# Performance work log

Measured on AMD Instinct MI355X. Metric: run time of the kernel, lower is better.

Reference implementation:

```python
import jax, jax.numpy as jnp
import numpy as np
import math

D_MODEL = 256
N_HEADS = 8
HEAD_DIM = D_MODEL // N_HEADS  # 32
N_LEVELS = 4
N_POINTS = 4
SHAPES = [(112, 112), (56, 56), (28, 28), (14, 14)]
LEN_IN = sum(h * w for h, w in SHAPES)  # 16660
BATCH = 1
LEN_Q = LEN_IN


def _grid_init_bias():
    # Faithful to MSDeformAttn._reset_parameters: directional grid init for sampling_offsets bias.
    thetas = np.arange(N_HEADS, dtype=np.float32) * (2.0 * math.pi / N_HEADS)
    grid = np.stack([np.cos(thetas), np.sin(thetas)], -1)
    grid = grid / np.abs(grid).max(-1, keepdims=True)
    grid = np.tile(grid[:, None, None, :], (1, N_LEVELS, N_POINTS, 1)).copy()
    for i in range(N_POINTS):
        grid[:, :, i, :] *= i + 1
    return jnp.asarray(grid.reshape(-1), dtype=jnp.float32)


def setup_inputs() -> dict:
    key = jax.random.key(0)
    ks = jax.random.split(key, 10)
    s = 1.0 / math.sqrt(D_MODEL)
    return {
        "query": jax.random.normal(ks[0], (BATCH, LEN_Q, D_MODEL), jnp.float32),
        "reference_points": jax.random.uniform(ks[1], (BATCH, LEN_Q, N_LEVELS, 2), jnp.float32),
        "input_flatten": jax.random.normal(ks[2], (BATCH, LEN_IN, D_MODEL), jnp.float32),
        "spatial_shapes": jnp.asarray(SHAPES, dtype=jnp.int32),
        "level_start_index": jnp.asarray(np.cumsum([0] + [h * w for h, w in SHAPES])[:-1], dtype=jnp.int32),
        "W_q": jax.random.normal(ks[3], (D_MODEL, D_MODEL), jnp.float32) * s,
        "b_q": jnp.zeros((D_MODEL,), jnp.float32),
        "W_k": jax.random.normal(ks[4], (D_MODEL, D_MODEL), jnp.float32) * s,
        "b_k": jnp.zeros((D_MODEL,), jnp.float32),
        "W_v": jax.random.normal(ks[5], (D_MODEL, D_MODEL), jnp.float32) * s,
        "b_v": jnp.zeros((D_MODEL,), jnp.float32),
        "W_o": jax.random.normal(ks[6], (D_MODEL, D_MODEL), jnp.float32) * s,
        "b_o": jnp.zeros((D_MODEL,), jnp.float32),
        "W_off": jax.random.normal(ks[7], (D_MODEL, N_HEADS * N_LEVELS * N_POINTS * 2), jnp.float32) * 0.01,
        "b_off": _grid_init_bias(),
    }


def _bilinear_sample(img, grid, H, W):
    # img: (B, H*W, D) flattened feature map; grid: (B, Q, P, 2) in [-1, 1] (x, y order).
    # Matches F.grid_sample(mode='bilinear', padding_mode='zeros', align_corners=False).
    B, Q, P, _ = grid.shape
    x = ((grid[..., 0] + 1.0) * W - 1.0) * 0.5
    y = ((grid[..., 1] + 1.0) * H - 1.0) * 0.5
    x0 = jnp.floor(x)
    y0 = jnp.floor(y)
    lx = x - x0
    ly = y - y0
    x0i = x0.astype(jnp.int32)
    y0i = y0.astype(jnp.int32)

    def gather(yi, xi, w):
        valid = (xi >= 0) & (xi < W) & (yi >= 0) & (yi < H)
        idx = jnp.clip(yi, 0, H - 1) * W + jnp.clip(xi, 0, W - 1)
        v = jnp.take_along_axis(img, idx.reshape(B, Q * P, 1), axis=1)
        return v.reshape(B, Q, P, -1) * (w * valid)[..., None]

    return (gather(y0i, x0i, (1.0 - ly) * (1.0 - lx))
            + gather(y0i, x0i + 1, (1.0 - ly) * lx)
            + gather(y0i + 1, x0i, ly * (1.0 - lx))
            + gather(y0i + 1, x0i + 1, ly * lx))


def reference(query, reference_points, input_flatten, spatial_shapes, level_start_index,
              W_q, b_q, W_k, b_k, W_v, b_v, W_o, b_o, W_off, b_off):
    N, Lq, C = query.shape
    M, D, L, P = N_HEADS, HEAD_DIM, N_LEVELS, N_POINTS

    q = query @ W_q + b_q                                   # (N, Lq, C)
    value = (input_flatten @ W_v + b_v).reshape(N, -1, M, D)
    key_h = (input_flatten @ W_k + b_k).reshape(N, -1, M, D)

    offsets = (q @ W_off + b_off).reshape(N, Lq, M, L, P, 2)
    # offset_normalizer = (W_l, H_l) per level
    norm = jnp.stack([spatial_shapes[:, 1], spatial_shapes[:, 0]], -1).astype(q.dtype)
    loc = reference_points[:, :, None, :, None, :] + offsets / norm[None, None, None, :, None, :]
    grids = 2.0 * loc - 1.0                                  # (N, Lq, M, L, P, 2)

    samp_v, samp_k = [], []
    start = 0
    for lid, (H, W) in enumerate(SHAPES):
        end = start + H * W
        v_l = value[:, start:end].transpose(0, 2, 1, 3).reshape(N * M, H * W, D)
        k_l = key_h[:, start:end].transpose(0, 2, 1, 3).reshape(N * M, H * W, D)
        g_l = grids[:, :, :, lid].transpose(0, 2, 1, 3, 4).reshape(N * M, Lq, P, 2)
        samp_v.append(_bilinear_sample(v_l, g_l, H, W))      # (N*M, Lq, P, D)
        samp_k.append(_bilinear_sample(k_l, g_l, H, W))
        start = end

    v_s = jnp.stack(samp_v, axis=2).reshape(N, M, Lq, L, P, D)
    k_s = jnp.stack(samp_k, axis=2).reshape(N, M, Lq, L, P, D)

    qh = q.reshape(N, Lq, M, D)
    logits = jnp.einsum('nqmd,nmqlpd->nmqlp', qh, k_s) / math.sqrt(D)
    attn = jax.nn.softmax(logits.reshape(N, M, Lq, L * P), axis=-1).reshape(N, M, Lq, L, P)

    out = jnp.einsum('nmqlp,nmqlpd->nqmd', attn, v_s).reshape(N, Lq, C)
    return out @ W_o + b_o
```

## Files before the change

kernel.cpp:

```cpp
#include <hip/hip_runtime.h>
#include <hip/hip_bf16.h>
#include <math.h>

#define LEN_IN   16660
#define D_MODEL  256
#define N_HEADS  8

typedef __attribute__((ext_vector_type(8))) short short8v;
typedef __attribute__((ext_vector_type(4))) float f32x4;
typedef _Float16 f16x2 __attribute__((ext_vector_type(2)));
typedef _Float16 f16x8 __attribute__((ext_vector_type(8)));

__device__ __forceinline__ unsigned short f2h(float f) {
  union { unsigned short u; _Float16 h; } c;
  c.h = (_Float16)f;
  return c.u;
}
__device__ __forceinline__ float h2f(unsigned short u) {
  union { unsigned short u; _Float16 h; } c;
  c.u = u;
  return (float)c.h;
}
__device__ __forceinline__ f16x2 u2h(unsigned u) {
  union { unsigned u; f16x2 h; } c;
  c.u = u;
  return c.h;
}

__global__ __launch_bounds__(256) void mega_prep(
    const float* __restrict__ query, const float* __restrict__ inp,
    const float* __restrict__ Wq, const float* __restrict__ Wk,
    const float* __restrict__ Wv, const float* __restrict__ Woff,
    const float* __restrict__ Wo,
    const float* __restrict__ bq, const float* __restrict__ boff,
    unsigned short* __restrict__ q16, unsigned short* __restrict__ in16,
    unsigned short* __restrict__ Btq, unsigned short* __restrict__ Btk,
    unsigned short* __restrict__ Btv, unsigned short* __restrict__ Bto,
    unsigned short* __restrict__ Btqo, float* __restrict__ bqo) {
  int b = blockIdx.x;
  int tid = threadIdx.x;

  if (b < 2048) {
    const int nq = (LEN_IN * D_MODEL) / 4;
    int i = b * 256 + tid;
    const int stride = 2048 * 256;
    for (int qd = i; qd < nq; qd += stride) {
      float4 va = ((const float4*)query)[qd];
      ushort4 ha = {f2h(va.x), f2h(va.y), f2h(va.z), f2h(va.w)};
      ((ushort4*)q16)[qd] = ha;
      float4 vb = ((const float4*)inp)[qd];
      ushort4 hb = {f2h(vb.x), f2h(vb.y), f2h(vb.z), f2h(vb.w)};
      ((ushort4*)in16)[qd] = hb;
    }
    return;
  }

  if (b < 2128) {
    __shared__ float tile[64][65];
    int bb = b - 2048;
    int mat = bb >> 4, t = bb & 15;
    int ti = t >> 2, tj = t & 3;
    const float* W = (mat == 0) ? Wq : (mat == 1) ? Wk : (mat == 2) ? Wv
                   : (mat == 3) ? Woff : Wo;
    unsigned short* Bt = (mat == 0) ? Btq : (mat == 1) ? Btk : (mat == 2) ? Btv
                       : (mat == 3) ? nullptr : Bto;
    if (mat == 3) return;
    #pragma unroll
    for (int i = 0; i < 16; i++) {
      int idx = tid + i * 256;
      int kr = idx >> 6, nc = idx & 63;
      tile[kr][nc] = W[(size_t)(ti * 64 + kr) * 256 + tj * 64 + nc];
    }
    __syncthreads();
    #pragma unroll
    for (int i = 0; i < 16; i++) {
      int idx = tid + i * 256;
      int nr = idx >> 6, kc = idx & 63;
      Bt[(size_t)(tj * 64 + nr) * 256 + ti * 64 + kc] = f2h(tile[kc][nr]);
    }
    return;
  }

  if (b == 2128) {
    float s = boff[tid];
    for (int i = 0; i < 256; i++) s += bq[i] * Woff[(size_t)i * 256 + tid];
    bqo[tid] = s;
    return;
  }

  {
    const int P = 40;
    __shared__ short As[64 * P], Bs[64 * P];
    int t = b - 2129;
    int m0 = (t >> 2) * 64, n0 = (t & 3) * 64;
    int w = tid >> 6, l = tid & 63;
    int r = l & 15, g = l >> 4;
    int mi = (w >> 1) * 32, ni = (w & 1) * 32;
    int sm = tid >> 2, sp = tid & 3;
    int kr = tid >> 3, nc = (tid & 7) * 8;

    f32x4 acc[2][2];
    #pragma unroll
    for (int a = 0; a < 2; a++)
      #pragma unroll
      for (int c = 0; c < 2; c++) acc[a][c] = (f32x4){0.f, 0.f, 0.f, 0.f};

    for (int k0 = 0; k0 < 256; k0 += 32) {
      const float* src = Wq + (size_t)(m0 + sm) * 256 + k0 + sp * 8;
      float4 u0 = *(const float4*)src;
      float4 u1 = *(const float4*)(src + 4);
      f16x8 hv = {(_Float16)u0.x, (_Float16)u0.y, (_Float16)u0.z, (_Float16)u0.w,
                  (_Float16)u1.x, (_Float16)u1.y, (_Float16)u1.z, (_Float16)u1.w};
      *(f16x8*)&As[sm * P + sp * 8] = hv;
      const float* wsrc = Woff + (size_t)(k0 + kr) * 256 + n0 + nc;
      float4 w0 = *(const float4*)wsrc;
      float4 w1 = *(const float4*)(wsrc + 4);
      Bs[(nc + 0) * P + kr] = (short)f2h(w0.x);
      Bs[(nc + 1) * P + kr] = (short)f2h(w0.y);
      Bs[(nc + 2) * P + kr] = (short)f2h(w0.z);
      Bs[(nc + 3) * P + kr] = (short)f2h(w0.w);
      Bs[(nc + 4) * P + kr] = (short)f2h(w1.x);
      Bs[(nc + 5) * P + kr] = (short)f2h(w1.y);
      Bs[(nc + 6) * P + kr] = (short)f2h(w1.z);
      Bs[(nc + 7) * P + kr] = (short)f2h(w1.w);
      __syncthreads();
      f16x8 af[2], bf[2];
      #pragma unroll
      for (int a = 0; a < 2; a++)
        af[a] = *(f16x8*)&As[(mi + a * 16 + r) * P + g * 8];
      #pragma unroll
      for (int c = 0; c < 2; c++)
        bf[c] = *(f16x8*)&Bs[(ni + c * 16 + r) * P + g * 8];
      #pragma unroll
      for (int a = 0; a < 2; a++)
        #pragma unroll
        for (int c = 0; c < 2; c++)
          acc[a][c] = __builtin_amdgcn_mfma_f32_16x16x32_f16(af[a], bf[c], acc[a][c], 0, 0, 0);
      __syncthreads();
    }
    #pragma unroll
    for (int a = 0; a < 2; a++)
      #pragma unroll
      for (int c = 0; c < 2; c++) {
        int col = n0 + ni + c * 16 + r;
        #pragma unroll
        for (int i = 0; i < 4; i++) {
          int row = m0 + mi + a * 16 + g * 4 + i;
          Btqo[(size_t)col * 256 + row] = f2h(acc[a][c][i]);
        }
      }
  }
}

__global__ __launch_bounds__(256) void gemm_qkv(
    const unsigned short* __restrict__ q16, const unsigned short* __restrict__ in16,
    const unsigned short* __restrict__ Btq,
    const unsigned short* __restrict__ Btk,
    const unsigned short* __restrict__ Btv,
    const unsigned short* __restrict__ Btqo,
    const float* __restrict__ bq, const float* __restrict__ bk,
    const float* __restrict__ bv, const float* __restrict__ bqo,
    unsigned short* __restrict__ qp_out, unsigned* __restrict__ kv_out,
    unsigned short* __restrict__ offs_out, int M) {
  const int P = 72;
  __shared__ short As[128 * P], B1[64 * P], B2[64 * P];
  int z = blockIdx.z;
  const unsigned short* A = (z == 1) ? in16 : q16;
  const unsigned short* Bt1 = (z == 0) ? Btq : (z == 1) ? Btk : Btqo;
  int tid = threadIdx.x;
  int m0 = blockIdx.x * 128, n0 = blockIdx.y * 64;
  int w = tid >> 6, l = tid & 63;
  int r = l & 15, g = l >> 4;
  int mi = (w >> 1) * 64, ni = (w & 1) * 32;
  int arow = tid >> 1, ach = (tid & 1) * 32;
  int brow = tid >> 2, bch = (tid & 3) * 16;

  f32x4 acc1[4][2], acc2[4][2];
  #pragma unroll
  for (int a = 0; a < 4; a++)
    #pragma unroll
    for (int b = 0; b < 2; b++) {
      acc1[a][b] = (f32x4){0.f, 0.f, 0.f, 0.f};
      acc2[a][b] = (f32x4){0.f, 0.f, 0.f, 0.f};
    }

  for (int k0 = 0; k0 < 256; k0 += 64) {
    int gm = m0 + arow;
    short8v a0 = {0,0,0,0,0,0,0,0}, a1 = a0, a2 = a0, a3 = a0;
    if (gm < M) {
      const unsigned short* src = A + (size_t)gm * 256 + k0 + ach;
      a0 = *(const short8v*)src;
      a1 = *(const short8v*)(src + 8);
      a2 = *(const short8v*)(src + 16);
      a3 = *(const short8v*)(src + 24);
    }
    *(short8v*)&As[arow * P + ach] = a0;
    *(short8v*)&As[arow * P + ach + 8] = a1;
    *(short8v*)&As[arow * P + ach + 16] = a2;
    *(short8v*)&As[arow * P + ach + 24] = a3;
    {
      const unsigned short* bsrc = Bt1 + (size_t)(n0 + brow) * 256 + k0 + bch;
      *(short8v*)&B1[brow * P + bch] = *(const short8v*)bsrc;
      *(short8v*)&B1[brow * P + bch + 8] = *(const short8v*)(bsrc + 8);
    }
    if (z == 1) {
      const unsigned short* bsrc = Btv + (size_t)(n0 + brow) * 256 + k0 + bch;
      *(short8v*)&B2[brow * P + bch] = *(const short8v*)bsrc;
      *(short8v*)&B2[brow * P + bch + 8] = *(const short8v*)(bsrc + 8);
    }
    __syncthreads();

    f16x8 af[4][2], b1f[2][2], b2f[2][2];
    #pragma unroll
    for (int a = 0; a < 4; a++)
      #pragma unroll
      for (int ks = 0; ks < 2; ks++)
        af[a][ks] = *(f16x8*)&As[(mi + a * 16 + r) * P + ks * 32 + g * 8];
    #pragma unroll
    for (int b = 0; b < 2; b++)
      #pragma unroll
      for (int ks = 0; ks < 2; ks++)
        b1f[b][ks] = *(f16x8*)&B1[(ni + b * 16 + r) * P + ks * 32 + g * 8];
    if (z == 1) {
      #pragma unroll
      for (int b = 0; b < 2; b++)
        #pragma unroll
        for (int ks = 0; ks < 2; ks++)
          b2f[b][ks] = *(f16x8*)&B2[(ni + b * 16 + r) * P + ks * 32 + g * 8];
    }
    #pragma unroll
    for (int a = 0; a < 4; a++)
      #pragma unroll
      for (int b = 0; b < 2; b++)
        #pragma unroll
        for (int ks = 0; ks < 2; ks++) {
          acc1[a][b] = __builtin_amdgcn_mfma_f32_16x16x32_f16(af[a][ks], b1f[b][ks], acc1[a][b], 0, 0, 0);
          if (z == 1)
            acc2[a][b] = __builtin_amdgcn_mfma_f32_16x16x32_f16(af[a][ks], b2f[b][ks], acc2[a][b], 0, 0, 0);
        }
    __syncthreads();
  }

  #pragma unroll
  for (int a = 0; a < 4; a++)
    #pragma unroll
    for (int b = 0; b < 2; b++) {
      int col = n0 + ni + b * 16 + r;
      if (z == 0) {
        float bc = bq[col];
        #pragma unroll
        for (int i = 0; i < 4; i++) {
          int row = m0 + mi + a * 16 + g * 4 + i;
          if (row < M) qp_out[(size_t)row * 256 + col] = f2h(acc1[a][b][i] + bc);
        }
      } else if (z == 1) {
        float bkc = bk[col], bvc = bv[col];
        int hh = col >> 5, cc = col & 31;
        #pragma unroll
        for (int i = 0; i < 4; i++) {
          int row = m0 + mi + a * 16 + g * 4 + i;
          if (row < M) {
            unsigned kh = f2h(acc1[a][b][i] + bkc);
            unsigned vh = f2h(acc2[a][b][i] + bvc);
            kv_out[((size_t)hh * LEN_IN + row) * 32 + cc] = kh | (vh << 16);
          }
        }
      } else {
        float bc = bqo[col];
        #pragma unroll
        for (int i = 0; i < 4; i++) {
          int row = m0 + mi + a * 16 + g * 4 + i;
          if (row < M) offs_out[(size_t)row * 256 + col] = f2h(acc1[a][b][i] + bc);
        }
      }
    }
}

__global__ __launch_bounds__(256) void gemm_out(
    const unsigned short* __restrict__ A,
    const unsigned short* __restrict__ Bt,
    const float* __restrict__ bias, float* __restrict__ C, int M) {
  const int P = 72;
  __shared__ short As[128 * P], Bs[64 * P];
  int tid = threadIdx.x;
  int m0 = blockIdx.x * 128, n0 = blockIdx.y * 64;
  int w = tid >> 6, l = tid & 63;
  int r = l & 15, g = l >> 4;
  int mi = (w >> 1) * 64, ni = (w & 1) * 32;
  int arow = tid >> 1, ach = (tid & 1) * 32;
  int brow = tid >> 2, bch = (tid & 3) * 16;

  f32x4 acc[4][2];
  #pragma unroll
  for (int a = 0; a < 4; a++)
    #pragma unroll
    for (int b = 0; b < 2; b++) acc[a][b] = (f32x4){0.f, 0.f, 0.f, 0.f};

  for (int k0 = 0; k0 < 256; k0 += 64) {
    int gm = m0 + arow;
    short8v a0 = {0,0,0,0,0,0,0,0}, a1 = a0, a2 = a0, a3 = a0;
    if (gm < M) {
      const unsigned short* src = A + (size_t)gm * 256 + k0 + ach;
      a0 = *(const short8v*)src;
      a1 = *(const short8v*)(src + 8);
      a2 = *(const short8v*)(src + 16);
      a3 = *(const short8v*)(src + 24);
    }
    *(short8v*)&As[arow * P + ach] = a0;
    *(short8v*)&As[arow * P + ach + 8] = a1;
    *(short8v*)&As[arow * P + ach + 16] = a2;
    *(short8v*)&As[arow * P + ach + 24] = a3;
    const unsigned short* bsrc = Bt + (size_t)(n0 + brow) * 256 + k0 + bch;
    *(short8v*)&Bs[brow * P + bch] = *(const short8v*)bsrc;
    *(short8v*)&Bs[brow * P + bch + 8] = *(const short8v*)(bsrc + 8);
    __syncthreads();

    f16x8 af[4][2], bf[2][2];
    #pragma unroll
    for (int a = 0; a < 4; a++)
      #pragma unroll
      for (int ks = 0; ks < 2; ks++)
        af[a][ks] = *(f16x8*)&As[(mi + a * 16 + r) * P + ks * 32 + g * 8];
    #pragma unroll
    for (int b = 0; b < 2; b++)
      #pragma unroll
      for (int ks = 0; ks < 2; ks++)
        bf[b][ks] = *(f16x8*)&Bs[(ni + b * 16 + r) * P + ks * 32 + g * 8];
    #pragma unroll
    for (int a = 0; a < 4; a++)
      #pragma unroll
      for (int b = 0; b < 2; b++)
        #pragma unroll
        for (int ks = 0; ks < 2; ks++)
          acc[a][b] = __builtin_amdgcn_mfma_f32_16x16x32_f16(af[a][ks], bf[b][ks], acc[a][b], 0, 0, 0);
    __syncthreads();
  }
  #pragma unroll
  for (int a = 0; a < 4; a++)
    #pragma unroll
    for (int b = 0; b < 2; b++) {
      int col = n0 + ni + b * 16 + r;
      float bc = bias[col];
      #pragma unroll
      for (int i = 0; i < 4; i++) {
        int row = m0 + mi + a * 16 + g * 4 + i;
        if (row < M) C[(size_t)row * 256 + col] = acc[a][b][i] + bc;
      }
    }
}

__global__ __launch_bounds__(256) void sample_attn(
    const unsigned short* __restrict__ qp,
    const unsigned short* __restrict__ offs,
    const float* __restrict__ rp,
    const unsigned* __restrict__ kv,
    unsigned short* __restrict__ attn_out) {
  __shared__ float vbuf[4][16][36];

  int tid = threadIdx.x;
  int wslot = tid >> 6;
  int lane = tid & 63;
  int wid = blockIdx.x * 4 + wslot;
  int q = wid >> 3;
  int h = wid & 7;

  int pt = lane >> 2;
  int c8 = (lane & 3) * 8;
  int l5 = lane & 31;

  float offv = h2f(offs[(size_t)q * 256 + h * 32 + l5]);
  float rpv = (l5 < 8) ? rp[(size_t)q * 8 + l5] : 0.f;

  int l = pt >> 2, pp = pt & 3;
  int W = 112 >> l;
  int start = (int)((50176u - (50176u >> (2 * l))) / 3u);

  float off_x = __shfl(offv, l * 8 + pp * 2 + 0, 32);
  float off_y = __shfl(offv, l * 8 + pp * 2 + 1, 32);
  float rp_x = __shfl(rpv, l * 2 + 0, 32);
  float rp_y = __shfl(rpv, l * 2 + 1, 32);

  float x = rp_x * (float)W + off_x - 0.5f;
  float y = rp_y * (float)W + off_y - 0.5f;
  float x0f = floorf(x), y0f = floorf(y);
  float lx = x - x0f, ly = y - y0f;
  int x0 = (int)x0f, y0 = (int)y0f;
  float wx0 = 1.f - lx, wy0 = 1.f - ly;
  float tw[4] = {wy0 * wx0, wy0 * lx, ly * wx0, ly * lx};

  const unsigned* kvh = kv + (size_t)h * LEN_IN * 32 + c8;

  f16x2 acc[8];
  #pragma unroll
  for (int j = 0; j < 8; j++) acc[j] = (f16x2){(_Float16)0.f, (_Float16)0.f};

  #pragma unroll
  for (int tap = 0; tap < 4; tap++) {
    int yy = y0 + (tap >> 1), xx = x0 + (tap & 1);
    bool valid = ((unsigned)xx < (unsigned)W) & ((unsigned)yy < (unsigned)W);
    float wgt = valid ? tw[tap] : 0.f;
    int pix = valid ? (start + yy * W + xx) : start;
    const unsigned* p = kvh + (size_t)pix * 32;
    uint4 u0 = *(const uint4*)p;
    uint4 u1 = *(const uint4*)(p + 4);
    _Float16 wh = (_Float16)wgt;
    f16x2 w2 = {wh, wh};
    acc[0] += w2 * u2h(u0.x);
    acc[1] += w2 * u2h(u0.y);
    acc[2] += w2 * u2h(u0.z);
    acc[3] += w2 * u2h(u0.w);
    acc[4] += w2 * u2h(u1.x);
    acc[5] += w2 * u2h(u1.y);
    acc[6] += w2 * u2h(u1.z);
    acc[7] += w2 * u2h(u1.w);
  }

  uint4 qa = *(const uint4*)(qp + (size_t)q * 256 + h * 32 + c8);
  float dot = 0.f;
  f16x2 kp;
  kp[0] = acc[0][0]; kp[1] = acc[1][0];
  dot = __builtin_amdgcn_fdot2(u2h(qa.x), kp, dot, false);
  kp[0] = acc[2][0]; kp[1] = acc[3][0];
  dot = __builtin_amdgcn_fdot2(u2h(qa.y), kp, dot, false);
  kp[0] = acc[4][0]; kp[1] = acc[5][0];
  dot = __builtin_amdgcn_fdot2(u2h(qa.z), kp, dot, false);
  kp[0] = acc[6][0]; kp[1] = acc[7][0];
  dot = __builtin_amdgcn_fdot2(u2h(qa.w), kp, dot, false);
  dot += __shfl_xor(dot, 1, 64);
  dot += __shfl_xor(dot, 2, 64);

  float e = __expf(dot * 0.17677669529663687f);
  float s = e;
  s += __shfl_xor(s, 4, 64);
  s += __shfl_xor(s, 8, 64);
  s += __shfl_xor(s, 16, 64);
  s += __shfl_xor(s, 32, 64);
  float wsc = e / s;

  float4 v0 = {wsc * (float)acc[0][1], wsc * (float)acc[1][1],
               wsc * (float)acc[2][1], wsc * (float)acc[3][1]};
  float4 v1 = {wsc * (float)acc[4][1], wsc * (float)acc[5][1],
               wsc * (float)acc[6][1], wsc * (float)acc[7][1]};
  *(float4*)&vbuf[wslot][pt][c8] = v0;
  *(float4*)&vbuf[wslot][pt][c8 + 4] = v1;
  __syncthreads();

  if (lane < 32) {
    float o = 0.f;
    #pragma unroll
    for (int p = 0; p < 16; p++) o += vbuf[wslot][p][lane];
    attn_out[(size_t)q * 256 + h * 32 + lane] = f2h(o);
  }
}

extern "C" void kernel_launch(void* const* d_in, const int* in_sizes, int n_in,
                              void* d_out, int out_size, void* d_ws, size_t ws_size,
                              hipStream_t stream) {
  const float* query = (const float*)d_in[0];
  const float* rp    = (const float*)d_in[1];
  const float* inp   = (const float*)d_in[2];
  const float* W_q   = (const float*)d_in[5];
  const float* b_q   = (const float*)d_in[6];
  const float* W_k   = (const float*)d_in[7];
  const float* b_k   = (const float*)d_in[8];
  const float* W_v   = (const float*)d_in[9];
  const float* b_v   = (const float*)d_in[10];
  const float* W_o   = (const float*)d_in[11];
  const float* b_o   = (const float*)d_in[12];
  const float* W_off = (const float*)d_in[13];
  const float* b_off = (const float*)d_in[14];
  float* out = (float*)d_out;

  const size_t nelem = (size_t)LEN_IN * D_MODEL;
  unsigned short* q16   = (unsigned short*)d_ws;
  unsigned short* in16  = q16 + nelem;
  unsigned short* qp    = in16 + nelem;
  unsigned short* offsb = qp + nelem;
  unsigned short* attn  = offsb + nelem;
  unsigned* kvp = (unsigned*)(attn + nelem);
  unsigned short* Btq   = (unsigned short*)(kvp + nelem);
  unsigned short* Btk   = Btq + 256 * 256;
  unsigned short* Btv   = Btk + 256 * 256;
  unsigned short* Bto   = Btv + 256 * 256;
  unsigned short* Btqo  = Bto + 256 * 256;
  float* bqo = (float*)(Btqo + 256 * 256);

  dim3 blk(256);
  dim3 ggrid((LEN_IN + 127) / 128, D_MODEL / 64);
  dim3 ggrid3((LEN_IN + 127) / 128, D_MODEL / 64, 3);

  mega_prep<<<2145, blk, 0, stream>>>(query, inp, W_q, W_k, W_v, W_off, W_o,
                                      b_q, b_off, q16, in16,
                                      Btq, Btk, Btv, Bto, Btqo, bqo);

  gemm_qkv<<<ggrid3, blk, 0, stream>>>(q16, in16, Btq, Btk, Btv, Btqo,
                                       b_q, b_k, b_v, bqo,
                                       qp, kvp, offsb, LEN_IN);

  int n_blocks = LEN_IN * N_HEADS / 4;
  sample_attn<<<n_blocks, blk, 0, stream>>>(qp, offsb, rp, kvp, attn);

  gemm_out<<<ggrid, blk, 0, stream>>>(attn, Bto, b_o, out, LEN_IN);
}
```

Measured before the change: 119.7 us.

## Fuse query fp16 conversion into GEMM and merge Q/offset projections

Drops the separate query fp32-to-fp16 conversion pass. The query tile is now loaded as fp32 and converted while it is staged into shared memory inside the GEMM. The Q and fused offset projections now share one A tile per block (z=0 computes both), so the grid shrinks from three z-slices to two and redundant A loads are removed. The sampling kernel also remaps block indices across queries and spreads the final 16-point reduction over all 64 lanes with a shuffle. In exchange, the z=0 blocks read twice as many bytes of A from global memory.

```diff
diff --git a/kernel.cpp b/kernel.cpp
--- a/kernel.cpp
+++ b/kernel.cpp
@@ -28,12 +28,12 @@
 }
 
 __global__ __launch_bounds__(256) void mega_prep(
-    const float* __restrict__ query, const float* __restrict__ inp,
+    const float* __restrict__ inp,
     const float* __restrict__ Wq, const float* __restrict__ Wk,
     const float* __restrict__ Wv, const float* __restrict__ Woff,
     const float* __restrict__ Wo,
     const float* __restrict__ bq, const float* __restrict__ boff,
-    unsigned short* __restrict__ q16, unsigned short* __restrict__ in16,
+    unsigned short* __restrict__ in16,
     unsigned short* __restrict__ Btq, unsigned short* __restrict__ Btk,
     unsigned short* __restrict__ Btv, unsigned short* __restrict__ Bto,
     unsigned short* __restrict__ Btqo, float* __restrict__ bqo) {
@@ -45,9 +45,6 @@
     int i = b * 256 + tid;
     const int stride = 2048 * 256;
     for (int qd = i; qd < nq; qd += stride) {
-      float4 va = ((const float4*)query)[qd];
-      ushort4 ha = {f2h(va.x), f2h(va.y), f2h(va.z), f2h(va.w)};
-      ((ushort4*)q16)[qd] = ha;
       float4 vb = ((const float4*)inp)[qd];
       ushort4 hb = {f2h(vb.x), f2h(vb.y), f2h(vb.z), f2h(vb.w)};
       ((ushort4*)in16)[qd] = hb;
@@ -60,11 +57,9 @@
     int bb = b - 2048;
     int mat = bb >> 4, t = bb & 15;
     int ti = t >> 2, tj = t & 3;
-    const float* W = (mat == 0) ? Wq : (mat == 1) ? Wk : (mat == 2) ? Wv
-                   : (mat == 3) ? Woff : Wo;
-    unsigned short* Bt = (mat == 0) ? Btq : (mat == 1) ? Btk : (mat == 2) ? Btv
-                       : (mat == 3) ? nullptr : Bto;
     if (mat == 3) return;
+    const float* W = (mat == 0) ? Wq : (mat == 1) ? Wk : (mat == 2) ? Wv : Wo;
+    unsigned short* Bt = (mat == 0) ? Btq : (mat == 1) ? Btk : (mat == 2) ? Btv : Bto;
     #pragma unroll
     for (int i = 0; i < 16; i++) {
       int idx = tid + i * 256;
@@ -153,7 +148,7 @@
 }
 
 __global__ __launch_bounds__(256) void gemm_qkv(
-    const unsigned short* __restrict__ q16, const unsigned short* __restrict__ in16,
+    const float* __restrict__ queryF, const unsigned short* __restrict__ in16,
     const unsigned short* __restrict__ Btq,
     const unsigned short* __restrict__ Btk,
     const unsigned short* __restrict__ Btv,
@@ -165,8 +160,8 @@
   const int P = 72;
   __shared__ short As[128 * P], B1[64 * P], B2[64 * P];
   int z = blockIdx.z;
-  const unsigned short* A = (z == 1) ? in16 : q16;
-  const unsigned short* Bt1 = (z == 0) ? Btq : (z == 1) ? Btk : Btqo;
+  const unsigned short* Bt1 = (z == 0) ? Btq : Btk;
+  const unsigned short* Bt2 = (z == 0) ? Btqo : Btv;
   int tid = threadIdx.x;
   int m0 = blockIdx.x * 128, n0 = blockIdx.y * 64;
   int w = tid >> 6, l = tid & 63;
@@ -186,27 +181,40 @@
 
   for (int k0 = 0; k0 < 256; k0 += 64) {
     int gm = m0 + arow;
-    short8v a0 = {0,0,0,0,0,0,0,0}, a1 = a0, a2 = a0, a3 = a0;
-    if (gm < M) {
-      const unsigned short* src = A + (size_t)gm * 256 + k0 + ach;
-      a0 = *(const short8v*)src;
-      a1 = *(const short8v*)(src + 8);
-      a2 = *(const short8v*)(src + 16);
-      a3 = *(const short8v*)(src + 24);
-    }
-    *(short8v*)&As[arow * P + ach] = a0;
-    *(short8v*)&As[arow * P + ach + 8] = a1;
-    *(short8v*)&As[arow * P + ach + 16] = a2;
-    *(short8v*)&As[arow * P + ach + 24] = a3;
+    if (z == 0) {
+      #pragma unroll
+      for (int t = 0; t < 4; t++) {
+        f16x8 hv = {0, 0, 0, 0, 0, 0, 0, 0};
+        if (gm < M) {
+          const float* src = queryF + (size_t)gm * 256 + k0 + ach + t * 8;
+          float4 u0 = *(const float4*)src;
+          float4 u1 = *(const float4*)(src + 4);
+          hv = (f16x8){(_Float16)u0.x, (_Float16)u0.y, (_Float16)u0.z, (_Float16)u0.w,
+                       (_Float16)u1.x, (_Float16)u1.y, (_Float16)u1.z, (_Float16)u1.w};
+        }
+        *(f16x8*)&As[arow * P + ach + t * 8] = hv;
+      }
+    } else {
+      short8v a0 = {0,0,0,0,0,0,0,0}, a1 = a0, a2 = a0, a3 = a0;
+      if (gm < M) {
+        const unsigned short* src = in16 + (size_t)gm * 256 + k0 + ach;
+        a0 = *(const short8v*)src;
+        a1 = *(const short8v*)(src + 8);
+        a2 = *(const short8v*)(src + 16);
+        a3 = *(const short8v*)(src + 24);
+      }
+      *(short8v*)&As[arow * P + ach] = a0;
+      *(short8v*)&As[arow * P + ach + 8] = a1;
+      *(short8v*)&As[arow * P + ach + 16] = a2;
+      *(short8v*)&As[arow * P + ach + 24] = a3;
+    }
     {
       const unsigned short* bsrc = Bt1 + (size_t)(n0 + brow) * 256 + k0 + bch;
       *(short8v*)&B1[brow * P + bch] = *(const short8v*)bsrc;
       *(short8v*)&B1[brow * P + bch + 8] = *(const short8v*)(bsrc + 8);
-    }
-    if (z == 1) {
-      const unsigned short* bsrc = Btv + (size_t)(n0 + brow) * 256 + k0 + bch;
-      *(short8v*)&B2[brow * P + bch] = *(const short8v*)bsrc;
-      *(short8v*)&B2[brow * P + bch + 8] = *(const short8v*)(bsrc + 8);
+      const unsigned short* bsrc2 = Bt2 + (size_t)(n0 + brow) * 256 + k0 + bch;
+      *(short8v*)&B2[brow * P + bch] = *(const short8v*)bsrc2;
+      *(short8v*)&B2[brow * P + bch + 8] = *(const short8v*)(bsrc2 + 8);
     }
     __syncthreads();
 
@@ -219,15 +227,10 @@
     #pragma unroll
     for (int b = 0; b < 2; b++)
       #pragma unroll
-      for (int ks = 0; ks < 2; ks++)
+      for (int ks = 0; ks < 2; ks++) {
         b1f[b][ks] = *(f16x8*)&B1[(ni + b * 16 + r) * P + ks * 32 + g * 8];
-    if (z == 1) {
-      #pragma unroll
-      for (int b = 0; b < 2; b++)
-        #pragma unroll
-        for (int ks = 0; ks < 2; ks++)
-          b2f[b][ks] = *(f16x8*)&B2[(ni + b * 16 + r) * P + ks * 32 + g * 8];
-    }
+        b2f[b][ks] = *(f16x8*)&B2[(ni + b * 16 + r) * P + ks * 32 + g * 8];
+      }
     #pragma unroll
     for (int a = 0; a < 4; a++)
       #pragma unroll
@@ -235,8 +238,7 @@
         #pragma unroll
         for (int ks = 0; ks < 2; ks++) {
           acc1[a][b] = __builtin_amdgcn_mfma_f32_16x16x32_f16(af[a][ks], b1f[b][ks], acc1[a][b], 0, 0, 0);
-          if (z == 1)
-            acc2[a][b] = __builtin_amdgcn_mfma_f32_16x16x32_f16(af[a][ks], b2f[b][ks], acc2[a][b], 0, 0, 0);
+          acc2[a][b] = __builtin_amdgcn_mfma_f32_16x16x32_f16(af[a][ks], b2f[b][ks], acc2[a][b], 0, 0, 0);
         }
     __syncthreads();
   }
@@ -247,13 +249,16 @@
     for (int b = 0; b < 2; b++) {
       int col = n0 + ni + b * 16 + r;
       if (z == 0) {
-        float bc = bq[col];
+        float bc1 = bq[col], bc2 = bqo[col];
         #pragma unroll
         for (int i = 0; i < 4; i++) {
           int row = m0 + mi + a * 16 + g * 4 + i;
-          if (row < M) qp_out[(size_t)row * 256 + col] = f2h(acc1[a][b][i] + bc);
+          if (row < M) {
+            qp_out[(size_t)row * 256 + col] = f2h(acc1[a][b][i] + bc1);
+            offs_out[(size_t)row * 256 + col] = f2h(acc2[a][b][i] + bc2);
+          }
         }
-      } else if (z == 1) {
+      } else {
         float bkc = bk[col], bvc = bv[col];
         int hh = col >> 5, cc = col & 31;
         #pragma unroll
@@ -264,13 +269,6 @@
             unsigned vh = f2h(acc2[a][b][i] + bvc);
             kv_out[((size_t)hh * LEN_IN + row) * 32 + cc] = kh | (vh << 16);
           }
-        }
-      } else {
-        float bc = bqo[col];
-        #pragma unroll
-        for (int i = 0; i < 4; i++) {
-          int row = m0 + mi + a * 16 + g * 4 + i;
-          if (row < M) offs_out[(size_t)row * 256 + col] = f2h(acc1[a][b][i] + bc);
         }
       }
     }
@@ -360,7 +358,9 @@
   int tid = threadIdx.x;
   int wslot = tid >> 6;
   int lane = tid & 63;
-  int wid = blockIdx.x * 4 + wslot;
+  int b = blockIdx.x;
+  int bs = (b & 7) * 4165 + (b >> 3);
+  int wid = bs * 4 + wslot;
   int q = wid >> 3;
   int h = wid & 7;
 
@@ -445,12 +445,14 @@
   *(float4*)&vbuf[wslot][pt][c8 + 4] = v1;
   __syncthreads();
 
-  if (lane < 32) {
-    float o = 0.f;
-    #pragma unroll
-    for (int p = 0; p < 16; p++) o += vbuf[wslot][p][lane];
-    attn_out[(size_t)q * 256 + h * 32 + lane] = f2h(o);
-  }
+  int half = lane >> 5;
+  int c = lane & 31;
+  float o = 0.f;
+  #pragma unroll
+  for (int p = 0; p < 8; p++) o += vbuf[wslot][half * 8 + p][c];
+  o += __shfl_xor(o, 32, 64);
+  if (lane < 32)
+    attn_out[(size_t)q * 256 + h * 32 + c] = f2h(o);
 }
 
 extern "C" void kernel_launch(void* const* d_in, const int* in_sizes, int n_in,
@@ -472,8 +474,7 @@
   float* out = (float*)d_out;
 
   const size_t nelem = (size_t)LEN_IN * D_MODEL;
-  unsigned short* q16   = (unsigned short*)d_ws;
-  unsigned short* in16  = q16 + nelem;
+  unsigned short* in16  = (unsigned short*)d_ws;
   unsigned short* qp    = in16 + nelem;
   unsigned short* offsb = qp + nelem;
   unsigned short* attn  = offsb + nelem;
@@ -487,13 +488,13 @@
 
   dim3 blk(256);
   dim3 ggrid((LEN_IN + 127) / 128, D_MODEL / 64);
-  dim3 ggrid3((LEN_IN + 127) / 128, D_MODEL / 64, 3);
-
-  mega_prep<<<2145, blk, 0, stream>>>(query, inp, W_q, W_k, W_v, W_off, W_o,
-                                      b_q, b_off, q16, in16,
+  dim3 ggrid2((LEN_IN + 127) / 128, D_MODEL / 64, 2);
+
+  mega_prep<<<2145, blk, 0, stream>>>(inp, W_q, W_k, W_v, W_off, W_o,
+                                      b_q, b_off, in16,
                                       Btq, Btk, Btv, Bto, Btqo, bqo);
 
-  gemm_qkv<<<ggrid3, blk, 0, stream>>>(q16, in16, Btq, Btk, Btv, Btqo,
+  gemm_qkv<<<ggrid2, blk, 0, stream>>>(query, in16, Btq, Btk, Btv, Btqo,
                                        b_q, b_k, b_v, bqo,
                                        qp, kvp, offsb, LEN_IN);
 
```

Measured after the change: 116.9 us. 2.3% less time.
